# Kernel optimization log

Measured on AMD Instinct MI355X. Metric: run time of the kernel, lower is better.

## Reference

```python
import jax, jax.numpy as jnp
import numpy as np

D = 128        # node_representation_size
V = 100000     # unique_internal_nodes (embedding vocab)
N = 20000      # nodes in the internal graph
E = 640000     # total neighbor (edge) entries


def setup_inputs() -> dict:
    key = jax.random.key(0)
    k1, k2, k3, k4, k5, k6 = jax.random.split(key, 6)
    node_ids = jax.random.randint(k1, (N,), 0, V)
    neighbor_ids = jax.random.randint(k2, (E,), 0, V)
    segment_ids = jnp.sort(jax.random.randint(k3, (E,), 0, N))
    xav = 1.0 / np.sqrt(D)  # xavier_normal std for square [D,D]
    W = jax.random.normal(k4, (D, D), dtype=jnp.float32) * xav
    M = jax.random.normal(k5, (D, D), dtype=jnp.float32) * xav
    emb = jax.random.normal(k6, (V, D), dtype=jnp.float32)
    return {"node_ids": node_ids, "neighbor_ids": neighbor_ids,
            "segment_ids": segment_ids, "W": W, "M": M, "emb": emb}


def reference(node_ids, neighbor_ids, segment_ids, W, M, emb):
    # Per node: s = relu(W @ e[node] + sum_{nbr} M @ e[nbr]); result = sum_nodes s
    self_term = emb[node_ids] @ W.T                       # [N, D]
    nb_msgs = emb[neighbor_ids] @ M.T                     # [E, D]
    nb_agg = jax.ops.segment_sum(nb_msgs, segment_ids, num_segments=N)  # [N, D]
    per_node = jax.nn.relu(self_term + nb_agg)            # [N, D]
    result = per_node.sum(axis=0)                         # [D]
    return jax.nn.softmax(result)[:, None]                # [D, 1], softmax over dim 0
```

## Files before the change

### kernel.cpp

```cpp
#include <hip/hip_runtime.h>

#define D 128
#define RS_STRIDE 64

typedef __attribute__((ext_vector_type(8))) short bf16x8;
typedef __attribute__((ext_vector_type(8))) unsigned short u16x8;
typedef __attribute__((ext_vector_type(4))) float f32x4;

__device__ __forceinline__ unsigned short f2bf(float f) {
    unsigned u = __float_as_uint(f);
    unsigned r = (u + 0x7fffu + ((u >> 16) & 1u)) >> 16;
    return (unsigned short)r;
}
__device__ __forceinline__ float bf2f(unsigned short h) {
    return __uint_as_float(((unsigned)h) << 16);
}
__device__ __forceinline__ ushort4 pack4(float4 v) {
    ushort4 o; o.x = f2bf(v.x); o.y = f2bf(v.y); o.z = f2bf(v.z); o.w = f2bf(v.w);
    return o;
}

__global__ void prep_kernel(const float* __restrict__ emb, const float* __restrict__ W,
                            const float* __restrict__ M, const int* __restrict__ seg,
                            unsigned short* __restrict__ embb, unsigned short* __restrict__ Wb,
                            unsigned short* __restrict__ Mb, float* __restrict__ rs,
                            int* __restrict__ row_ptr, int n4, int E, int N) {
    int i = blockIdx.x * blockDim.x + threadIdx.x;
    if (i < n4) ((ushort4*)embb)[i] = pack4(((const float4*)emb)[i]);
    if (i < 4096)       ((ushort4*)Wb)[i]        = pack4(((const float4*)W)[i]);
    else if (i < 8192)  ((ushort4*)Mb)[i - 4096] = pack4(((const float4*)M)[i - 4096]);
    if (i < D) rs[i * RS_STRIDE] = 0.0f;
    if (i < E) {
        int s = seg[i];
        if (i == 0) {
            for (int n = 0; n <= s; ++n) row_ptr[n] = 0;
        } else {
            int sp = seg[i - 1];
            for (int n = sp + 1; n <= s; ++n) row_ptr[n] = i;
        }
        if (i == E - 1) {
            for (int n = s + 1; n <= N; ++n) row_ptr[n] = E;
        }
    }
}

__global__ void agg_bf_kernel(const int* __restrict__ nbr, const int* __restrict__ row_ptr,
                              const unsigned short* __restrict__ embb,
                              unsigned short* __restrict__ aggb, int N) {
    int n = blockIdx.x * 4 + (threadIdx.x >> 6);
    if (n >= N) return;
    int tt = threadIdx.x & 63;
    int c = tt & 3;
    int j = tt >> 2;

    int lo = row_ptr[n], hi = row_ptr[n + 1];

    float s[4][8];
#pragma unroll
    for (int q = 0; q < 4; ++q)
#pragma unroll
        for (int k = 0; k < 8; ++k) s[q][k] = 0.f;

    int e = lo + j;
    int id = (e < hi) ? nbr[e] : -1;
    while (id >= 0) {
        const u16x8* r = (const u16x8*)(embb + (size_t)id * D);
        int e2 = e + 16;
        int id2 = (e2 < hi) ? nbr[e2] : -1;
        u16x8 v0 = r[c], v1 = r[c + 4], v2 = r[c + 8], v3 = r[c + 12];
#pragma unroll
        for (int k = 0; k < 8; ++k) {
            s[0][k] += bf2f((unsigned short)v0[k]);
            s[1][k] += bf2f((unsigned short)v1[k]);
            s[2][k] += bf2f((unsigned short)v2[k]);
            s[3][k] += bf2f((unsigned short)v3[k]);
        }
        e = e2; id = id2;
    }
#pragma unroll
    for (int q = 0; q < 4; ++q)
#pragma unroll
        for (int k = 0; k < 8; ++k) {
            float x = s[q][k];
            x += __shfl_xor(x, 4);
            x += __shfl_xor(x, 8);
            x += __shfl_xor(x, 16);
            x += __shfl_xor(x, 32);
            s[q][k] = x;
        }

    if (j == 0) {
        u16x8* o = (u16x8*)(aggb + (size_t)n * D);
#pragma unroll
        for (int q = 0; q < 4; ++q) {
            u16x8 ov;
#pragma unroll
            for (int k = 0; k < 8; ++k) ov[k] = f2bf(s[q][k]);
            o[c + 4 * q] = ov;
        }
    }
}

__global__ void agg_f32_kernel(const int* __restrict__ nbr, const int* __restrict__ row_ptr,
                               const float* __restrict__ emb,
                               unsigned short* __restrict__ aggb, int N) {
    int n = blockIdx.x * 4 + (threadIdx.x >> 6);
    if (n >= N) return;
    int tt = threadIdx.x & 63;
    int c = tt & 7;
    int j = tt >> 3;

    int lo = row_ptr[n], hi = row_ptr[n + 1];

    float4 s0 = make_float4(0.f, 0.f, 0.f, 0.f);
    float4 s1 = make_float4(0.f, 0.f, 0.f, 0.f);
    float4 s2 = make_float4(0.f, 0.f, 0.f, 0.f);
    float4 s3 = make_float4(0.f, 0.f, 0.f, 0.f);
    for (int e = lo + j; e < hi; e += 8) {
        const float4* r = (const float4*)&emb[(size_t)nbr[e] * D];
        float4 v0 = r[c], v1 = r[c + 8], v2 = r[c + 16], v3 = r[c + 24];
        s0.x += v0.x; s0.y += v0.y; s0.z += v0.z; s0.w += v0.w;
        s1.x += v1.x; s1.y += v1.y; s1.z += v1.z; s1.w += v1.w;
        s2.x += v2.x; s2.y += v2.y; s2.z += v2.z; s2.w += v2.w;
        s3.x += v3.x; s3.y += v3.y; s3.z += v3.z; s3.w += v3.w;
    }
#pragma unroll
    for (int o = 8; o <= 32; o <<= 1) {
        s0.x += __shfl_xor(s0.x, o); s0.y += __shfl_xor(s0.y, o);
        s0.z += __shfl_xor(s0.z, o); s0.w += __shfl_xor(s0.w, o);
        s1.x += __shfl_xor(s1.x, o); s1.y += __shfl_xor(s1.y, o);
        s1.z += __shfl_xor(s1.z, o); s1.w += __shfl_xor(s1.w, o);
        s2.x += __shfl_xor(s2.x, o); s2.y += __shfl_xor(s2.y, o);
        s2.z += __shfl_xor(s2.z, o); s2.w += __shfl_xor(s2.w, o);
        s3.x += __shfl_xor(s3.x, o); s3.y += __shfl_xor(s3.y, o);
        s3.z += __shfl_xor(s3.z, o); s3.w += __shfl_xor(s3.w, o);
    }
    if (j == 0) {
        ushort4* o = (ushort4*)(aggb + (size_t)n * D);
        o[c]      = pack4(s0);
        o[c + 8]  = pack4(s1);
        o[c + 16] = pack4(s2);
        o[c + 24] = pack4(s3);
    }
}

template <bool BF>
__global__ __launch_bounds__(256) void matvec_kernel(
    const int* __restrict__ node_ids, const void* __restrict__ embv,
    const unsigned short* __restrict__ aggb,
    const unsigned short* __restrict__ Wb, const unsigned short* __restrict__ Mb,
    float* __restrict__ rs, int N, int ngroups, int nstripes) {
    int t = threadIdx.x;
    int wid = blockIdx.x * 4 + (t >> 6);
    int l = t & 63;
    int quad = l >> 4, col = l & 15;
    int dt = wid & 7;
    int stripe = wid >> 3;

    bf16x8 bw[4], bm[4];
    int wrow = (dt * 16 + col) * D;
#pragma unroll
    for (int ks = 0; ks < 4; ++ks) {
        int off = wrow + ks * 32 + quad * 8;
        bw[ks] = *(const bf16x8*)(Wb + off);
        bm[ks] = *(const bf16x8*)(Mb + off);
    }

    const bf16x8 zero8 = {0, 0, 0, 0, 0, 0, 0, 0};
    float vsum = 0.f;

    for (int grp = stripe; grp < ngroups; grp += nstripes) {
        int node = grp * 16 + col;
        bool valid = node < N;
        int nid = valid ? node_ids[node] : 0;
        const unsigned short* ar = aggb + (size_t)node * D + quad * 8;

        f32x4 acc = {0.f, 0.f, 0.f, 0.f};
#pragma unroll
        for (int ks = 0; ks < 4; ++ks) {
            bf16x8 ax;
            if (BF) {
                const unsigned short* xr =
                    (const unsigned short*)embv + (size_t)nid * D + quad * 8;
                ax = valid ? *(const bf16x8*)(xr + ks * 32) : zero8;
            } else {
                if (valid) {
                    const float4* xf = (const float4*)((const float*)embv +
                                       (size_t)nid * D + quad * 8 + ks * 32);
                    ushort4 p0 = pack4(xf[0]);
                    ushort4 p1 = pack4(xf[1]);
                    ax[0] = (short)p0.x; ax[1] = (short)p0.y;
                    ax[2] = (short)p0.z; ax[3] = (short)p0.w;
                    ax[4] = (short)p1.x; ax[5] = (short)p1.y;
                    ax[6] = (short)p1.z; ax[7] = (short)p1.w;
                } else ax = zero8;
            }
            bf16x8 aa = valid ? *(const bf16x8*)(ar + ks * 32) : zero8;
            acc = __builtin_amdgcn_mfma_f32_16x16x32_bf16(ax, bw[ks], acc, 0, 0, 0);
            acc = __builtin_amdgcn_mfma_f32_16x16x32_bf16(aa, bm[ks], acc, 0, 0, 0);
        }
        vsum += fmaxf(acc[0], 0.f) + fmaxf(acc[1], 0.f)
              + fmaxf(acc[2], 0.f) + fmaxf(acc[3], 0.f);
    }

    vsum += __shfl_xor(vsum, 16);
    vsum += __shfl_xor(vsum, 32);
    if (l < 16) atomicAdd(&rs[(dt * 16 + col) * RS_STRIDE], vsum);
}

__global__ void softmax_kernel(const float* __restrict__ rs, float* __restrict__ out) {
    int t = threadIdx.x;
    float v0 = rs[t * RS_STRIDE];
    float v1 = rs[(t + 64) * RS_STRIDE];
    float m = fmaxf(v0, v1);
    for (int o = 32; o > 0; o >>= 1) m = fmaxf(m, __shfl_xor(m, o));
    float e0 = expf(v0 - m);
    float e1 = expf(v1 - m);
    float s = e0 + e1;
    for (int o = 32; o > 0; o >>= 1) s += __shfl_xor(s, o);
    float inv = 1.0f / s;
    out[t] = e0 * inv;
    out[t + 64] = e1 * inv;
}

extern "C" void kernel_launch(void* const* d_in, const int* in_sizes, int n_in,
                              void* d_out, int out_size, void* d_ws, size_t ws_size,
                              hipStream_t stream) {
    const int*   node_ids = (const int*)d_in[0];
    const int*   nbr      = (const int*)d_in[1];
    const int*   seg      = (const int*)d_in[2];
    const float* W        = (const float*)d_in[3];
    const float* M        = (const float*)d_in[4];
    const float* emb      = (const float*)d_in[5];
    float* out = (float*)d_out;

    int N = in_sizes[0];
    int E = in_sizes[1];
    long long VD = in_sizes[5];
    int ngroups  = (N + 15) / 16;
    int nstripes = (ngroups + 1) / 2;
    int mv_blocks = 2 * nstripes;

    unsigned short* aggb = (unsigned short*)d_ws;
    unsigned short* Wb   = aggb + (size_t)N * D;
    unsigned short* Mb   = Wb + D * D;
    float* rs            = (float*)(Mb + D * D);
    int* row_ptr         = (int*)(rs + (size_t)D * RS_STRIDE);
    unsigned short* embb = (unsigned short*)(row_ptr + (N + 1));

    size_t need_bf = (size_t)(row_ptr + (N + 1) - (int*)d_ws) * 4 + (size_t)VD * 2;
    bool use_bf = ws_size >= need_bf;
    int n4 = use_bf ? (int)(VD / 4) : 0;
    int prep_n = n4;
    if (prep_n < E) prep_n = E;
    if (prep_n < 8192) prep_n = 8192;

    prep_kernel<<<(prep_n + 255) / 256, 256, 0, stream>>>(emb, W, M, seg, embb, Wb, Mb,
                                                          rs, row_ptr, n4, E, N);
    if (use_bf) {
        agg_bf_kernel<<<(N + 3) / 4, 256, 0, stream>>>(nbr, row_ptr, embb, aggb, N);
        matvec_kernel<true><<<mv_blocks, 256, 0, stream>>>(node_ids, embb, aggb, Wb, Mb,
                                                           rs, N, ngroups, nstripes);
    } else {
        agg_f32_kernel<<<(N + 3) / 4, 256, 0, stream>>>(nbr, row_ptr, emb, aggb, N);
        matvec_kernel<false><<<mv_blocks, 256, 0, stream>>>(node_ids, emb, aggb, Wb, Mb,
                                                            rs, N, ngroups, nstripes);
    }
    softmax_kernel<<<1, 64, 0, stream>>>(rs, out);
}
```

Measured before the change: 155.3 us.

## Fuse aggregation, matvec and softmax into one kernel with LDS staging

Merges the neighbor aggregation, the MFMA matvec with ReLU-sum, and the softmax into a single kernel. Each block handles 16 nodes, stages their embeddings and bf16 aggregates in swizzled shared memory, and runs the MFMA directly, so the aggb round trip through global memory and two launches go away. The last block to finish, detected with an atomic counter, computes the softmax. In exchange it drops the fp32 fallback path, assumes the workspace always fits the bf16 embedding copy, reloads W and M in every block, and does many more atomics into rs.

```diff
diff --git a/kernel.cpp b/kernel.cpp
--- a/kernel.cpp
+++ b/kernel.cpp
@@ -24,12 +24,14 @@
                             const float* __restrict__ M, const int* __restrict__ seg,
                             unsigned short* __restrict__ embb, unsigned short* __restrict__ Wb,
                             unsigned short* __restrict__ Mb, float* __restrict__ rs,
-                            int* __restrict__ row_ptr, int n4, int E, int N) {
+                            int* __restrict__ row_ptr, int* __restrict__ done,
+                            int n4, int E, int N) {
     int i = blockIdx.x * blockDim.x + threadIdx.x;
     if (i < n4) ((ushort4*)embb)[i] = pack4(((const float4*)emb)[i]);
     if (i < 4096)       ((ushort4*)Wb)[i]        = pack4(((const float4*)W)[i]);
     else if (i < 8192)  ((ushort4*)Mb)[i - 4096] = pack4(((const float4*)M)[i - 4096]);
     if (i < D) rs[i * RS_STRIDE] = 0.0f;
+    if (i == D) *done = 0;
     if (i < E) {
         int s = seg[i];
         if (i == 0) {
@@ -44,16 +46,37 @@
     }
 }
 
-__global__ void agg_bf_kernel(const int* __restrict__ nbr, const int* __restrict__ row_ptr,
-                              const unsigned short* __restrict__ embb,
-                              unsigned short* __restrict__ aggb, int N) {
-    int n = blockIdx.x * 4 + (threadIdx.x >> 6);
-    if (n >= N) return;
-    int tt = threadIdx.x & 63;
-    int c = tt & 3;
-    int j = tt >> 2;
-
-    int lo = row_ptr[n], hi = row_ptr[n + 1];
+__global__ __launch_bounds__(256) void fused_kernel(
+    const int* __restrict__ node_ids, const int* __restrict__ nbr,
+    const int* __restrict__ row_ptr, const unsigned short* __restrict__ embb,
+    const unsigned short* __restrict__ Wb, const unsigned short* __restrict__ Mb,
+    float* __restrict__ rs, int* __restrict__ done, float* __restrict__ out,
+    int N, int nblocks) {
+    __shared__ u16x8 xs4[256];
+    __shared__ u16x8 as4[256];
+    __shared__ int amlast;
+
+    int t = threadIdx.x;
+    int wave = t >> 6, tt = t & 63;
+    int nb = blockIdx.x << 4;
+
+    int ns  = tt >> 4;
+    int n15 = (wave << 2) + ns;
+    int n   = nb + n15;
+    bool nvalid = n < N;
+
+    int c2 = tt & 15;
+    const u16x8 z8 = {0, 0, 0, 0, 0, 0, 0, 0};
+    u16x8 xv = z8;
+    if (nvalid) {
+        int nid = node_ids[n];
+        xv = *((const u16x8*)(embb + (size_t)nid * D) + c2);
+    }
+
+    int jj = (tt >> 2) & 3;
+    int cc = tt & 3;
+    int lo = 0, hi = 0;
+    if (nvalid) { lo = row_ptr[n]; hi = row_ptr[n + 1]; }
 
     float s[4][8];
 #pragma unroll
@@ -61,13 +84,13 @@
 #pragma unroll
         for (int k = 0; k < 8; ++k) s[q][k] = 0.f;
 
-    int e = lo + j;
+    int e = lo + jj;
     int id = (e < hi) ? nbr[e] : -1;
     while (id >= 0) {
         const u16x8* r = (const u16x8*)(embb + (size_t)id * D);
-        int e2 = e + 16;
+        int e2 = e + 4;
         int id2 = (e2 < hi) ? nbr[e2] : -1;
-        u16x8 v0 = r[c], v1 = r[c + 4], v2 = r[c + 8], v3 = r[c + 12];
+        u16x8 v0 = r[cc], v1 = r[cc + 4], v2 = r[cc + 8], v3 = r[cc + 12];
 #pragma unroll
         for (int k = 0; k < 8; ++k) {
             s[0][k] += bf2f((unsigned short)v0[k]);
@@ -84,143 +107,67 @@
             float x = s[q][k];
             x += __shfl_xor(x, 4);
             x += __shfl_xor(x, 8);
-            x += __shfl_xor(x, 16);
-            x += __shfl_xor(x, 32);
             s[q][k] = x;
         }
 
-    if (j == 0) {
-        u16x8* o = (u16x8*)(aggb + (size_t)n * D);
+    xs4[(n15 << 4) + (c2 ^ n15)] = xv;
+    if (jj == 0) {
 #pragma unroll
         for (int q = 0; q < 4; ++q) {
+            int chunk = cc + (q << 2);
             u16x8 ov;
 #pragma unroll
             for (int k = 0; k < 8; ++k) ov[k] = f2bf(s[q][k]);
-            o[c + 4 * q] = ov;
-        }
-    }
-}
-
-__global__ void agg_f32_kernel(const int* __restrict__ nbr, const int* __restrict__ row_ptr,
-                               const float* __restrict__ emb,
-                               unsigned short* __restrict__ aggb, int N) {
-    int n = blockIdx.x * 4 + (threadIdx.x >> 6);
-    if (n >= N) return;
-    int tt = threadIdx.x & 63;
-    int c = tt & 7;
-    int j = tt >> 3;
-
-    int lo = row_ptr[n], hi = row_ptr[n + 1];
-
-    float4 s0 = make_float4(0.f, 0.f, 0.f, 0.f);
-    float4 s1 = make_float4(0.f, 0.f, 0.f, 0.f);
-    float4 s2 = make_float4(0.f, 0.f, 0.f, 0.f);
-    float4 s3 = make_float4(0.f, 0.f, 0.f, 0.f);
-    for (int e = lo + j; e < hi; e += 8) {
-        const float4* r = (const float4*)&emb[(size_t)nbr[e] * D];
-        float4 v0 = r[c], v1 = r[c + 8], v2 = r[c + 16], v3 = r[c + 24];
-        s0.x += v0.x; s0.y += v0.y; s0.z += v0.z; s0.w += v0.w;
-        s1.x += v1.x; s1.y += v1.y; s1.z += v1.z; s1.w += v1.w;
-        s2.x += v2.x; s2.y += v2.y; s2.z += v2.z; s2.w += v2.w;
-        s3.x += v3.x; s3.y += v3.y; s3.z += v3.z; s3.w += v3.w;
-    }
-#pragma unroll
-    for (int o = 8; o <= 32; o <<= 1) {
-        s0.x += __shfl_xor(s0.x, o); s0.y += __shfl_xor(s0.y, o);
-        s0.z += __shfl_xor(s0.z, o); s0.w += __shfl_xor(s0.w, o);
-        s1.x += __shfl_xor(s1.x, o); s1.y += __shfl_xor(s1.y, o);
-        s1.z += __shfl_xor(s1.z, o); s1.w += __shfl_xor(s1.w, o);
-        s2.x += __shfl_xor(s2.x, o); s2.y += __shfl_xor(s2.y, o);
-        s2.z += __shfl_xor(s2.z, o); s2.w += __shfl_xor(s2.w, o);
-        s3.x += __shfl_xor(s3.x, o); s3.y += __shfl_xor(s3.y, o);
-        s3.z += __shfl_xor(s3.z, o); s3.w += __shfl_xor(s3.w, o);
-    }
-    if (j == 0) {
-        ushort4* o = (ushort4*)(aggb + (size_t)n * D);
-        o[c]      = pack4(s0);
-        o[c + 8]  = pack4(s1);
-        o[c + 16] = pack4(s2);
-        o[c + 24] = pack4(s3);
-    }
-}
-
-template <bool BF>
-__global__ __launch_bounds__(256) void matvec_kernel(
-    const int* __restrict__ node_ids, const void* __restrict__ embv,
-    const unsigned short* __restrict__ aggb,
-    const unsigned short* __restrict__ Wb, const unsigned short* __restrict__ Mb,
-    float* __restrict__ rs, int N, int ngroups, int nstripes) {
-    int t = threadIdx.x;
-    int wid = blockIdx.x * 4 + (t >> 6);
-    int l = t & 63;
-    int quad = l >> 4, col = l & 15;
-    int dt = wid & 7;
-    int stripe = wid >> 3;
-
-    bf16x8 bw[4], bm[4];
-    int wrow = (dt * 16 + col) * D;
-#pragma unroll
-    for (int ks = 0; ks < 4; ++ks) {
-        int off = wrow + ks * 32 + quad * 8;
-        bw[ks] = *(const bf16x8*)(Wb + off);
-        bm[ks] = *(const bf16x8*)(Mb + off);
-    }
-
-    const bf16x8 zero8 = {0, 0, 0, 0, 0, 0, 0, 0};
-    float vsum = 0.f;
-
-    for (int grp = stripe; grp < ngroups; grp += nstripes) {
-        int node = grp * 16 + col;
-        bool valid = node < N;
-        int nid = valid ? node_ids[node] : 0;
-        const unsigned short* ar = aggb + (size_t)node * D + quad * 8;
-
+            as4[(n15 << 4) + (chunk ^ n15)] = ov;
+        }
+    }
+    __syncthreads();
+
+    int quad = tt >> 4, col = tt & 15;
+#pragma unroll
+    for (int s2 = 0; s2 < 2; ++s2) {
+        int dt = (wave << 1) + s2;
+        const unsigned short* wr = Wb + ((dt * 16 + col) * D + quad * 8);
+        const unsigned short* mr = Mb + ((dt * 16 + col) * D + quad * 8);
         f32x4 acc = {0.f, 0.f, 0.f, 0.f};
 #pragma unroll
         for (int ks = 0; ks < 4; ++ks) {
-            bf16x8 ax;
-            if (BF) {
-                const unsigned short* xr =
-                    (const unsigned short*)embv + (size_t)nid * D + quad * 8;
-                ax = valid ? *(const bf16x8*)(xr + ks * 32) : zero8;
-            } else {
-                if (valid) {
-                    const float4* xf = (const float4*)((const float*)embv +
-                                       (size_t)nid * D + quad * 8 + ks * 32);
-                    ushort4 p0 = pack4(xf[0]);
-                    ushort4 p1 = pack4(xf[1]);
-                    ax[0] = (short)p0.x; ax[1] = (short)p0.y;
-                    ax[2] = (short)p0.z; ax[3] = (short)p0.w;
-                    ax[4] = (short)p1.x; ax[5] = (short)p1.y;
-                    ax[6] = (short)p1.z; ax[7] = (short)p1.w;
-                } else ax = zero8;
-            }
-            bf16x8 aa = valid ? *(const bf16x8*)(ar + ks * 32) : zero8;
-            acc = __builtin_amdgcn_mfma_f32_16x16x32_bf16(ax, bw[ks], acc, 0, 0, 0);
-            acc = __builtin_amdgcn_mfma_f32_16x16x32_bf16(aa, bm[ks], acc, 0, 0, 0);
-        }
-        vsum += fmaxf(acc[0], 0.f) + fmaxf(acc[1], 0.f)
-              + fmaxf(acc[2], 0.f) + fmaxf(acc[3], 0.f);
-    }
-
-    vsum += __shfl_xor(vsum, 16);
-    vsum += __shfl_xor(vsum, 32);
-    if (l < 16) atomicAdd(&rs[(dt * 16 + col) * RS_STRIDE], vsum);
-}
-
-__global__ void softmax_kernel(const float* __restrict__ rs, float* __restrict__ out) {
-    int t = threadIdx.x;
-    float v0 = rs[t * RS_STRIDE];
-    float v1 = rs[(t + 64) * RS_STRIDE];
-    float m = fmaxf(v0, v1);
-    for (int o = 32; o > 0; o >>= 1) m = fmaxf(m, __shfl_xor(m, o));
-    float e0 = expf(v0 - m);
-    float e1 = expf(v1 - m);
-    float s = e0 + e1;
-    for (int o = 32; o > 0; o >>= 1) s += __shfl_xor(s, o);
-    float inv = 1.0f / s;
-    out[t] = e0 * inv;
-    out[t + 64] = e1 * inv;
+            bf16x8 bw = *(const bf16x8*)(wr + ks * 32);
+            bf16x8 bm = *(const bf16x8*)(mr + ks * 32);
+            int p = (col << 4) + ((quad + (ks << 2)) ^ col);
+            bf16x8 ax = *(const bf16x8*)&xs4[p];
+            bf16x8 aa = *(const bf16x8*)&as4[p];
+            acc = __builtin_amdgcn_mfma_f32_16x16x32_bf16(ax, bw, acc, 0, 0, 0);
+            acc = __builtin_amdgcn_mfma_f32_16x16x32_bf16(aa, bm, acc, 0, 0, 0);
+        }
+        float v = fmaxf(acc[0], 0.f) + fmaxf(acc[1], 0.f)
+                + fmaxf(acc[2], 0.f) + fmaxf(acc[3], 0.f);
+        v += __shfl_xor(v, 16);
+        v += __shfl_xor(v, 32);
+        if (tt < 16) atomicAdd(&rs[(dt * 16 + col) * RS_STRIDE], v);
+    }
+
+    __threadfence();
+    if (t == 0) amlast = (atomicAdd(done, 1) == nblocks - 1);
+    __syncthreads();
+    if (amlast) {
+        __threadfence();
+        if (t < 64) {
+            float v0 = __hip_atomic_load(&rs[t * RS_STRIDE],
+                                         __ATOMIC_RELAXED, __HIP_MEMORY_SCOPE_AGENT);
+            float v1 = __hip_atomic_load(&rs[(t + 64) * RS_STRIDE],
+                                         __ATOMIC_RELAXED, __HIP_MEMORY_SCOPE_AGENT);
+            float m = fmaxf(v0, v1);
+            for (int o = 32; o > 0; o >>= 1) m = fmaxf(m, __shfl_xor(m, o));
+            float e0 = expf(v0 - m);
+            float e1 = expf(v1 - m);
+            float su = e0 + e1;
+            for (int o = 32; o > 0; o >>= 1) su += __shfl_xor(su, o);
+            float inv = 1.0f / su;
+            out[t] = e0 * inv;
+            out[t + 64] = e1 * inv;
+        }
+    }
 }
 
 extern "C" void kernel_launch(void* const* d_in, const int* in_sizes, int n_in,
@@ -237,34 +184,22 @@
     int N = in_sizes[0];
     int E = in_sizes[1];
     long long VD = in_sizes[5];
-    int ngroups  = (N + 15) / 16;
-    int nstripes = (ngroups + 1) / 2;
-    int mv_blocks = 2 * nstripes;
-
-    unsigned short* aggb = (unsigned short*)d_ws;
-    unsigned short* Wb   = aggb + (size_t)N * D;
+    int nblocks = (N + 15) / 16;
+
+    unsigned short* embb = (unsigned short*)d_ws;
+    unsigned short* Wb   = embb + (size_t)VD;
     unsigned short* Mb   = Wb + D * D;
     float* rs            = (float*)(Mb + D * D);
     int* row_ptr         = (int*)(rs + (size_t)D * RS_STRIDE);
-    unsigned short* embb = (unsigned short*)(row_ptr + (N + 1));
-
-    size_t need_bf = (size_t)(row_ptr + (N + 1) - (int*)d_ws) * 4 + (size_t)VD * 2;
-    bool use_bf = ws_size >= need_bf;
-    int n4 = use_bf ? (int)(VD / 4) : 0;
+    int* done            = row_ptr + (N + 1);
+
+    int n4 = (int)(VD / 4);
     int prep_n = n4;
     if (prep_n < E) prep_n = E;
     if (prep_n < 8192) prep_n = 8192;
 
     prep_kernel<<<(prep_n + 255) / 256, 256, 0, stream>>>(emb, W, M, seg, embb, Wb, Mb,
-                                                          rs, row_ptr, n4, E, N);
-    if (use_bf) {
-        agg_bf_kernel<<<(N + 3) / 4, 256, 0, stream>>>(nbr, row_ptr, embb, aggb, N);
-        matvec_kernel<true><<<mv_blocks, 256, 0, stream>>>(node_ids, embb, aggb, Wb, Mb,
-                                                           rs, N, ngroups, nstripes);
-    } else {
-        agg_f32_kernel<<<(N + 3) / 4, 256, 0, stream>>>(nbr, row_ptr, emb, aggb, N);
-        matvec_kernel<false><<<mv_blocks, 256, 0, stream>>>(node_ids, emb, aggb, Wb, Mb,
-                                                            rs, N, ngroups, nstripes);
-    }
-    softmax_kernel<<<1, 64, 0, stream>>>(rs, out);
-}
+                                                          rs, row_ptr, done, n4, E, N);
+    fused_kernel<<<nblocks, 256, 0, stream>>>(node_ids, nbr, row_ptr, embb, Wb, Mb,
+                                              rs, done, out, N, nblocks);
+}
```

Measured after the change: 226.0 us. 1.46x slower.
